# Kernel tuning notes

Hardware: AMD Instinct MI355X
Metric: run time of the kernel (lower is better)

Reference implementation:

```python
import jax, jax.numpy as jnp
import numpy as np

B = 8192
NUM_NODES = 100000
EMB = 128
W1D, W2D, W3D = 64, 128, 256   # witness_dims
CODE = 128
HID = 64                        # hardcoded hidden_dim in WitnessExtractor / decoder
TOTW = W1D + W2D + W3D          # 448


def _linear_params(key, fan_in, fan_out):
    k1, k2 = jax.random.split(key)
    bound = 1.0 / np.sqrt(fan_in)
    w = jax.random.uniform(k1, (fan_out, fan_in), jnp.float32, -bound, bound)
    b = jax.random.uniform(k2, (fan_out,), jnp.float32, -bound, bound)
    return w, b


def setup_inputs() -> dict:
    key = jax.random.key(0)
    ks = jax.random.split(key, 12)
    u = jax.random.randint(ks[0], (B,), 0, NUM_NODES, dtype=jnp.int64 if jax.config.jax_enable_x64 else jnp.int32)
    v = jax.random.randint(ks[1], (B,), 0, NUM_NODES, dtype=u.dtype)
    emb = jax.random.normal(ks[2], (NUM_NODES, EMB), jnp.float32)
    e1_w1, e1_b1 = _linear_params(ks[3], 2 * EMB, HID)
    e1_w2, e1_b2 = _linear_params(ks[4], HID, W1D)
    e2_w1, e2_b1 = _linear_params(ks[5], 2 * EMB + W1D, HID)
    e2_w2, e2_b2 = _linear_params(ks[6], HID, W2D)
    e3_w1, e3_b1 = _linear_params(ks[7], 2 * EMB + W2D, HID)
    e3_w2, e3_b2 = _linear_params(ks[8], HID, W3D)
    trop_w = jax.random.normal(ks[9], (CODE, TOTW), jnp.float32)  # init_scale=1.0
    dec_w1, dec_b1 = _linear_params(ks[10], CODE, HID)
    dec_w2, dec_b2 = _linear_params(ks[11], HID, 1)
    return dict(u=u, v=v, emb=emb,
                e1_w1=e1_w1, e1_b1=e1_b1, e1_w2=e1_w2, e1_b2=e1_b2,
                e2_w1=e2_w1, e2_b1=e2_b1, e2_w2=e2_w2, e2_b2=e2_b2,
                e3_w1=e3_w1, e3_b1=e3_b1, e3_w2=e3_w2, e3_b2=e3_b2,
                trop_w=trop_w, dec_w1=dec_w1, dec_b1=dec_b1,
                dec_w2=dec_w2, dec_b2=dec_b2)


def _witness(x, w1, b1, w2, b2):
    h = jax.nn.relu(x @ w1.T + b1)
    return jax.nn.sigmoid(h @ w2.T + b2)


def reference(u, v, emb,
              e1_w1, e1_b1, e1_w2, e1_b2,
              e2_w1, e2_b1, e2_w2, e2_b2,
              e3_w1, e3_b1, e3_w2, e3_b2,
              trop_w, dec_w1, dec_b1, dec_w2, dec_b2):
    u_emb = emb[u]                               # [B, EMB]
    v_emb = emb[v]
    base = jnp.concatenate([u_emb, v_emb], axis=1)  # [B, 2*EMB]
    w1 = _witness(base, e1_w1, e1_b1, e1_w2, e1_b2)
    w2 = _witness(jnp.concatenate([base, w1], axis=1), e2_w1, e2_b1, e2_w2, e2_b2)
    w3 = _witness(jnp.concatenate([base, w2], axis=1), e3_w1, e3_b1, e3_w2, e3_b2)
    wit = jnp.concatenate([w1, w2, w3], axis=1)  # [B, TOTW]
    # tropical (min-plus) matmul: code[b,o] = min_j (wit[b,j] + trop_w[o,j])
    code = jnp.min(wit[:, None, :] + trop_w[None, :, :], axis=2)  # [B, CODE]
    h = jax.nn.relu(code @ dec_w1.T + dec_b1)
    return h @ dec_w2.T + dec_b2                 # [B, 1]
```

## Files before the change

kernel.cpp:

```cpp
#include <hip/hip_runtime.h>
#include <hip/hip_fp16.h>
#include <math.h>

#define BATCH 8192
#define EMB 128
#define TILE 16
#define NTHREADS 1024
#define NWAVES 16
#define CH 136
#define WITS 450
#define ENT_CAP 4096

#define OFF_E1W1 0
#define OFF_E1W2 16384
#define OFF_E2W1 20480
#define OFF_E2W2 40960
#define OFF_E3W1 49152
#define OFF_E3W2 73728
#define OFF_DW1  90112
#define OFF_DW2  98304
#define W_DENSE  98368

typedef __attribute__((ext_vector_type(8))) _Float16 v8h;
typedef __attribute__((ext_vector_type(4))) float v4f;

struct Smem {
    _Float16 XB[32 * CH];
    _Float16 W12C[24 * CH];
    _Float16 H[8 * CH];
    _Float16 CODE[16 * CH];
    _Float16 WITrm[TILE * WITS];
    unsigned int ent[ENT_CAP];
    unsigned int off[132];
};

__global__ __launch_bounds__(1024) void prep_kernel(
    const float* __restrict__ s0, const float* __restrict__ s1,
    const float* __restrict__ s2, const float* __restrict__ s3,
    const float* __restrict__ s4, const float* __restrict__ s5,
    const float* __restrict__ s6, const float* __restrict__ s7,
    const float* __restrict__ trop, _Float16* __restrict__ ws)
{
    const int b = blockIdx.x;
    const int tid = threadIdx.x;
    if (b < 25) {
        const int idx4 = (b * 1024 + tid) * 4;
        if (idx4 >= W_DENSE) return;
        const float* src; int off;
        if      (idx4 < OFF_E1W2) { src = s0; off = OFF_E1W1; }
        else if (idx4 < OFF_E2W1) { src = s1; off = OFF_E1W2; }
        else if (idx4 < OFF_E2W2) { src = s2; off = OFF_E2W1; }
        else if (idx4 < OFF_E3W1) { src = s3; off = OFF_E2W2; }
        else if (idx4 < OFF_E3W2) { src = s4; off = OFF_E3W1; }
        else if (idx4 < OFF_DW1)  { src = s5; off = OFF_E3W2; }
        else if (idx4 < OFF_DW2)  { src = s6; off = OFF_DW1;  }
        else                      { src = s7; off = OFF_DW2;  }
        const float4 v = *(const float4*)(src + (idx4 - off));
        _Float16* dst = ws + idx4;
        dst[0] = (_Float16)v.x; dst[1] = (_Float16)v.y;
        dst[2] = (_Float16)v.z; dst[3] = (_Float16)v.w;
    } else {
        __shared__ float thrs[128];
        __shared__ unsigned int cnt[128];
        __shared__ unsigned int offs[129];
        const int lane = tid & 63;
        const int wave = tid >> 6;

        for (int o = wave; o < 128; o += 16) {
            const float* row = trop + (size_t)o * 448;
            float vals[7];
            float mn = 1e30f;
            #pragma unroll
            for (int it = 0; it < 7; ++it) {
                vals[it] = row[lane + it * 64];
                mn = fminf(mn, vals[it]);
            }
            mn = fminf(mn, __shfl_xor(mn, 1, 64));
            mn = fminf(mn, __shfl_xor(mn, 2, 64));
            mn = fminf(mn, __shfl_xor(mn, 4, 64));
            mn = fminf(mn, __shfl_xor(mn, 8, 64));
            mn = fminf(mn, __shfl_xor(mn, 16, 64));
            mn = fminf(mn, __shfl_xor(mn, 32, 64));
            const float thr = mn + 1.02f;
            int n = 0;
            #pragma unroll
            for (int it = 0; it < 7; ++it)
                n += __popcll(__ballot(vals[it] <= thr));
            if (lane == 0) { thrs[o] = thr; cnt[o] = (unsigned)n; }
        }
        __syncthreads();

        if (tid == 0) {
            unsigned int s = 0;
            for (int i = 0; i < 128; ++i) { offs[i] = s; s += cnt[i]; }
            offs[128] = s;
        }
        __syncthreads();

        unsigned int* base = (unsigned int*)(ws + W_DENSE);
        if (tid < 129) base[tid] = offs[tid];

        for (int o = wave; o < 128; o += 16) {
            const float* row = trop + (size_t)o * 448;
            const float thr = thrs[o];
            unsigned int done = offs[o];
            #pragma unroll
            for (int it = 0; it < 7; ++it) {
                const int j = lane + it * 64;
                const float t = row[j];
                const bool p = (t <= thr);
                const unsigned long long m = __ballot(p);
                if (p) {
                    const unsigned int pos =
                        done + (unsigned)__popcll(m & ((1ull << lane) - 1ull));
                    if (pos < ENT_CAP) {
                        const unsigned short hb =
                            __builtin_bit_cast(unsigned short, (_Float16)t);
                        base[132 + pos] = ((unsigned)j << 16) | hb;
                    }
                }
                done += (unsigned)__popcll(m);
            }
        }
    }
}

template <int K, int STEPS0, int O, int ACT, bool CHUNKW, bool RMW>
__device__ __forceinline__ void dense_mfma(
    const _Float16* __restrict__ Wg, const float* __restrict__ bias,
    const _Float16* A0, const _Float16* A1,
    _Float16* OutC, _Float16* OutRM, int rmbase, int wave, int lane)
{
    constexpr int STEPS = K / 32;
    constexpr int NJOBS = O / 16;
    const int l15 = lane & 15;
    const int quad = lane >> 4;

    for (int nt = wave; nt < NJOBS; nt += NWAVES) {
        v4f c = {0.f, 0.f, 0.f, 0.f};
        const _Float16* wrow = Wg + (size_t)(nt * 16 + l15) * K + quad * 8;
        #pragma unroll
        for (int s = 0; s < STEPS; ++s) {
            const int g = s * 4 + quad;
            const _Float16* asrc = (s < STEPS0)
                ? (A0 + g * CH + l15 * 8)
                : (A1 + (g - STEPS0 * 4) * CH + l15 * 8);
            const v8h a = *(const v8h*)asrc;
            const v8h bfr = *(const v8h*)(wrow + s * 32);
            c = __builtin_amdgcn_mfma_f32_16x16x32_f16(a, bfr, c, 0, 0, 0);
        }
        const int o = nt * 16 + l15;
        const float bs = bias[o];
        #pragma unroll
        for (int i = 0; i < 4; ++i) {
            float vv = c[i] + bs;
            if (ACT == 0) vv = fmaxf(vv, 0.f);
            else          vv = 1.f / (1.f + __expf(-vv));
            const int m = quad * 4 + i;
            const _Float16 hv = (_Float16)vv;
            if (CHUNKW) OutC[(o >> 3) * CH + m * 8 + (o & 7)] = hv;
            if (RMW)    OutRM[m * WITS + rmbase + o] = hv;
        }
    }
}

__global__ __launch_bounds__(NTHREADS, 8) void tacit_fused_kernel(
    const int* __restrict__ u, const int* __restrict__ v,
    const float* __restrict__ emb,
    const float* __restrict__ e1_b1, const float* __restrict__ e1_b2,
    const float* __restrict__ e2_b1, const float* __restrict__ e2_b2,
    const float* __restrict__ e3_b1, const float* __restrict__ e3_b2,
    const float* __restrict__ dec_b1, const float* __restrict__ dec_b2,
    const _Float16* __restrict__ ws,
    float* __restrict__ out)
{
    __shared__ Smem S;
    const int tid = threadIdx.x;
    const int lane = tid & 63;
    const int wave = tid >> 6;
    const int row0 = blockIdx.x * TILE;

    if (tid < 512) {
        const int row = tid & 15;
        const int kq = tid >> 4;
        const int node = (kq < 16) ? u[row0 + row] : v[row0 + row];
        const int col = (kq & 15) * 8;
        const float4 f0 = *(const float4*)(emb + (size_t)node * EMB + col);
        const float4 f1 = *(const float4*)(emb + (size_t)node * EMB + col + 4);
        v8h hv;
        hv[0] = (_Float16)f0.x; hv[1] = (_Float16)f0.y;
        hv[2] = (_Float16)f0.z; hv[3] = (_Float16)f0.w;
        hv[4] = (_Float16)f1.x; hv[5] = (_Float16)f1.y;
        hv[6] = (_Float16)f1.z; hv[7] = (_Float16)f1.w;
        *(v8h*)&S.XB[kq * CH + row * 8] = hv;
    }
    {
        const unsigned int* base = (const unsigned int*)(ws + W_DENSE);
        if (tid < 33) *(uint4*)&S.off[tid * 4] = *(const uint4*)(base + tid * 4);
        *(uint4*)&S.ent[tid * 4] = *(const uint4*)(base + 132 + tid * 4);
    }
    __syncthreads();

    dense_mfma<256, 8, 64, 0, true, false>(ws + OFF_E1W1, e1_b1, S.XB, nullptr,
                                           S.H, nullptr, 0, wave, lane);
    __syncthreads();
    dense_mfma<64, 2, 64, 1, true, true>(ws + OFF_E1W2, e1_b2, S.H, nullptr,
                                         S.W12C, S.WITrm, 0, wave, lane);
    __syncthreads();

    dense_mfma<320, 8, 64, 0, true, false>(ws + OFF_E2W1, e2_b1, S.XB, S.W12C,
                                           S.H, nullptr, 0, wave, lane);
    __syncthreads();
    dense_mfma<64, 2, 128, 1, true, true>(ws + OFF_E2W2, e2_b2, S.H, nullptr,
                                          S.W12C + 8 * CH, S.WITrm, 64, wave, lane);
    __syncthreads();

    dense_mfma<384, 8, 64, 0, true, false>(ws + OFF_E3W1, e3_b1, S.XB, S.W12C + 8 * CH,
                                           S.H, nullptr, 0, wave, lane);
    __syncthreads();
    dense_mfma<64, 2, 256, 1, false, true>(ws + OFF_E3W2, e3_b2, S.H, nullptr,
                                           nullptr, S.WITrm, 192, wave, lane);
    __syncthreads();

    {
        const int r = lane & 15;
        const int cp = lane >> 4;
        const _Float16* wrow = &S.WITrm[r * WITS];
        #pragma unroll
        for (int i = 0; i < 8; ++i) {
            const int o = (wave << 3) + i;
            const int beg = (int)S.off[o];
            const int end = (int)S.off[o + 1];
            float acc = 1e30f;
            for (int idx = beg + cp; idx < end; idx += 4) {
                const unsigned int cwv = S.ent[idx];
                const int j = (int)(cwv >> 16);
                const float tv = (float)__builtin_bit_cast(
                    _Float16, (unsigned short)(cwv & 0xffffu));
                acc = fminf(acc, (float)wrow[j] + tv);
            }
            acc = fminf(acc, __shfl_xor(acc, 16, 64));
            acc = fminf(acc, __shfl_xor(acc, 32, 64));
            if (cp == 0)
                S.CODE[(o >> 3) * CH + r * 8 + (o & 7)] = (_Float16)acc;
        }
    }
    __syncthreads();

    dense_mfma<128, 4, 64, 0, true, false>(ws + OFF_DW1, dec_b1, S.CODE, nullptr,
                                           S.H, nullptr, 0, wave, lane);
    __syncthreads();

    if (tid < TILE) {
        const int r = tid;
        float s = dec_b2[0];
        const _Float16* w2 = ws + OFF_DW2;
        #pragma unroll
        for (int c = 0; c < 8; ++c) {
            const v8h hr = *(const v8h*)(&S.H[c * CH + r * 8]);
            const v8h wr = *(const v8h*)(w2 + c * 8);
            #pragma unroll
            for (int t = 0; t < 8; ++t) s += (float)hr[t] * (float)wr[t];
        }
        out[row0 + r] = s;
    }
}

extern "C" void kernel_launch(void* const* d_in, const int* in_sizes, int n_in,
                              void* d_out, int out_size, void* d_ws, size_t ws_size,
                              hipStream_t stream) {
    const int*   u      = (const int*)d_in[0];
    const int*   v      = (const int*)d_in[1];
    const float* emb    = (const float*)d_in[2];
    const float* e1_w1  = (const float*)d_in[3];
    const float* e1_b1  = (const float*)d_in[4];
    const float* e1_w2  = (const float*)d_in[5];
    const float* e1_b2  = (const float*)d_in[6];
    const float* e2_w1  = (const float*)d_in[7];
    const float* e2_b1  = (const float*)d_in[8];
    const float* e2_w2  = (const float*)d_in[9];
    const float* e2_b2  = (const float*)d_in[10];
    const float* e3_w1  = (const float*)d_in[11];
    const float* e3_b1  = (const float*)d_in[12];
    const float* e3_w2  = (const float*)d_in[13];
    const float* e3_b2  = (const float*)d_in[14];
    const float* trop_w = (const float*)d_in[15];
    const float* dec_w1 = (const float*)d_in[16];
    const float* dec_b1 = (const float*)d_in[17];
    const float* dec_w2 = (const float*)d_in[18];
    const float* dec_b2 = (const float*)d_in[19];
    float* out = (float*)d_out;
    _Float16* ws = (_Float16*)d_ws;

    prep_kernel<<<26, 1024, 0, stream>>>(
        e1_w1, e1_w2, e2_w1, e2_w2, e3_w1, e3_w2, dec_w1, dec_w2, trop_w, ws);

    tacit_fused_kernel<<<BATCH / TILE, NTHREADS, 0, stream>>>(
        u, v, emb,
        e1_b1, e1_b2, e2_b1, e2_b2, e3_b1, e3_b2, dec_b1, dec_b2,
        ws, out);
}
```

Measured before the change: 157.6 us.

## Parallelize tropical sparse-list build across blocks using atomic offset allocation

The tropical weight sparsification in the prep kernel is spread over 8 blocks, one wave per output row, instead of a single block. Slots are handed out with a global atomicAdd counter in place of a serial prefix scan with two syncthreads and a second pass over global memory. Each row stores its count and start packed into one word, and the fused kernel decodes it and clamps the end to ENT_CAP. This adds a memset launch to reset the counter and makes entry order depend on the atomic order, which does not affect the min result.

After: 147.6 us. 6.3% less time.

```diff
diff --git a/kernel.cpp b/kernel.cpp
--- a/kernel.cpp
+++ b/kernel.cpp
@@ -60,67 +60,55 @@
         dst[0] = (_Float16)v.x; dst[1] = (_Float16)v.y;
         dst[2] = (_Float16)v.z; dst[3] = (_Float16)v.w;
     } else {
-        __shared__ float thrs[128];
-        __shared__ unsigned int cnt[128];
-        __shared__ unsigned int offs[129];
         const int lane = tid & 63;
         const int wave = tid >> 6;
-
-        for (int o = wave; o < 128; o += 16) {
-            const float* row = trop + (size_t)o * 448;
-            float vals[7];
-            float mn = 1e30f;
-            #pragma unroll
-            for (int it = 0; it < 7; ++it) {
-                vals[it] = row[lane + it * 64];
-                mn = fminf(mn, vals[it]);
+        const int o = (b - 25) * 16 + wave;
+        if (o >= 128) return;
+        unsigned int* base = (unsigned int*)(ws + W_DENSE);
+        unsigned int* counter = base + 131;
+
+        const float* row = trop + (size_t)o * 448;
+        float vals[7];
+        float mn = 1e30f;
+        #pragma unroll
+        for (int it = 0; it < 7; ++it) {
+            vals[it] = row[lane + it * 64];
+            mn = fminf(mn, vals[it]);
+        }
+        mn = fminf(mn, __shfl_xor(mn, 1, 64));
+        mn = fminf(mn, __shfl_xor(mn, 2, 64));
+        mn = fminf(mn, __shfl_xor(mn, 4, 64));
+        mn = fminf(mn, __shfl_xor(mn, 8, 64));
+        mn = fminf(mn, __shfl_xor(mn, 16, 64));
+        mn = fminf(mn, __shfl_xor(mn, 32, 64));
+        const float thr = mn + 1.02f;
+
+        unsigned long long masks[7];
+        unsigned int n = 0;
+        #pragma unroll
+        for (int it = 0; it < 7; ++it) {
+            masks[it] = __ballot(vals[it] <= thr);
+            n += (unsigned)__popcll(masks[it]);
+        }
+        unsigned int beg = 0;
+        if (lane == 0) beg = atomicAdd(counter, n);
+        beg = (unsigned)__shfl((int)beg, 0, 64);
+        if (lane == 0) base[o] = (n << 16) | (beg & 0xffffu);
+
+        unsigned int done = beg;
+        const unsigned long long ltmask = (1ull << lane) - 1ull;
+        #pragma unroll
+        for (int it = 0; it < 7; ++it) {
+            const unsigned long long m = masks[it];
+            if (vals[it] <= thr) {
+                const unsigned int pos = done + (unsigned)__popcll(m & ltmask);
+                if (pos < ENT_CAP) {
+                    const unsigned short hb =
+                        __builtin_bit_cast(unsigned short, (_Float16)vals[it]);
+                    base[132 + pos] = ((unsigned)(lane + it * 64) << 16) | hb;
+                }
             }
-            mn = fminf(mn, __shfl_xor(mn, 1, 64));
-            mn = fminf(mn, __shfl_xor(mn, 2, 64));
-            mn = fminf(mn, __shfl_xor(mn, 4, 64));
-            mn = fminf(mn, __shfl_xor(mn, 8, 64));
-            mn = fminf(mn, __shfl_xor(mn, 16, 64));
-            mn = fminf(mn, __shfl_xor(mn, 32, 64));
-            const float thr = mn + 1.02f;
-            int n = 0;
-            #pragma unroll
-            for (int it = 0; it < 7; ++it)
-                n += __popcll(__ballot(vals[it] <= thr));
-            if (lane == 0) { thrs[o] = thr; cnt[o] = (unsigned)n; }
-        }
-        __syncthreads();
-
-        if (tid == 0) {
-            unsigned int s = 0;
-            for (int i = 0; i < 128; ++i) { offs[i] = s; s += cnt[i]; }
-            offs[128] = s;
-        }
-        __syncthreads();
-
-        unsigned int* base = (unsigned int*)(ws + W_DENSE);
-        if (tid < 129) base[tid] = offs[tid];
-
-        for (int o = wave; o < 128; o += 16) {
-            const float* row = trop + (size_t)o * 448;
-            const float thr = thrs[o];
-            unsigned int done = offs[o];
-            #pragma unroll
-            for (int it = 0; it < 7; ++it) {
-                const int j = lane + it * 64;
-                const float t = row[j];
-                const bool p = (t <= thr);
-                const unsigned long long m = __ballot(p);
-                if (p) {
-                    const unsigned int pos =
-                        done + (unsigned)__popcll(m & ((1ull << lane) - 1ull));
-                    if (pos < ENT_CAP) {
-                        const unsigned short hb =
-                            __builtin_bit_cast(unsigned short, (_Float16)t);
-                        base[132 + pos] = ((unsigned)j << 16) | hb;
-                    }
-                }
-                done += (unsigned)__popcll(m);
-            }
+            done += (unsigned)__popcll(m);
         }
     }
 }
@@ -229,8 +217,10 @@
         #pragma unroll
         for (int i = 0; i < 8; ++i) {
             const int o = (wave << 3) + i;
-            const int beg = (int)S.off[o];
-            const int end = (int)S.off[o + 1];
+            const unsigned int tb = S.off[o];
+            const int beg = (int)(tb & 0xffffu);
+            int end = beg + (int)(tb >> 16);
+            end = end < ENT_CAP ? end : ENT_CAP;
             float acc = 1e30f;
             for (int idx = beg + cp; idx < end; idx += 4) {
                 const unsigned int cwv = S.ent[idx];
@@ -292,7 +282,9 @@
     float* out = (float*)d_out;
     _Float16* ws = (_Float16*)d_ws;
 
-    prep_kernel<<<26, 1024, 0, stream>>>(
+    hipMemsetAsync((char*)d_ws + (size_t)W_DENSE * 2 + 131 * 4, 0, 4, stream);
+
+    prep_kernel<<<33, 1024, 0, stream>>>(
         e1_w1, e1_w2, e2_w1, e2_w2, e3_w1, e3_w2, dec_w1, dec_w2, trop_w, ws);
 
     tacit_fused_kernel<<<BATCH / TILE, NTHREADS, 0, stream>>>(
```
